# Kernel optimization log

Measured on AMD Instinct MI355X. Metric: run time of the kernel, lower is better.

The kernel has to match this reference:

```python
import jax, jax.numpy as jnp
import numpy as np

SMALL_CONST = 1e-8
K = 128
N = 512 * 512  # pixels


def setup_inputs() -> dict:
    key = jax.random.key(0)
    ks = jax.random.split(key, 6)
    pos = jax.random.uniform(ks[0], (N, 2), jnp.float32, 0.0, 512.0)      # pixel coords
    mu = jax.random.uniform(ks[1], (K, 2), jnp.float32, 0.0, 512.0)       # gaussian centers
    alpha = jax.random.uniform(ks[2], (K,), jnp.float32)                   # opacities in [0,1]
    color = jax.random.uniform(ks[3], (K, 3), jnp.float32, 0.0, 255.0)     # RGB in [0,255]
    scales = 10.0 + jax.random.uniform(ks[4], (K, 2), jnp.float32) * 20.0  # anisotropic scales
    thetas = jax.random.uniform(ks[5], (K,), jnp.float32, -np.pi, np.pi)   # rotations
    return dict(pos=pos, mu=mu, alpha=alpha, color=color, scales=scales, thetas=thetas)


def _forward(pos, mu, alpha, color, scales, thetas):
    # Parameter clamps done at the top of the torch forward
    alpha = jnp.clip(alpha, 0.0, 1.0)
    color = jnp.clip(color, 0.0, 255.0)
    scales = jnp.clip(scales, 0.1, None)

    # Precompute all K inverse covariances: sigma_inv = R diag(1/s^2) R^T  -> [K,2,2]
    c, s = jnp.cos(thetas), jnp.sin(thetas)
    R = jnp.stack([jnp.stack([c, -s], -1), jnp.stack([s, c], -1)], -2)  # [K,2,2]
    inv2 = 1.0 / scales ** 2                                            # [K,2]
    sigma_inv = jnp.einsum('kti,ki,kji->ktj', R, inv2, R)               # [K,2,2]

    n = pos.shape[0]
    pc0 = jnp.zeros((n, 3), pos.dtype)
    pa0 = jnp.zeros((n, 1), pos.dtype)

    def step(carry, g):
        pc, pa = carry
        mu_k, si_k, a_k, col_k = g
        diff = pos - mu_k                                          # [N,2]
        expo = -0.5 * jnp.einsum('ni,ij,nj->n', diff, si_k, diff)  # [N]
        alpha_k = (a_k * jnp.exp(expo))[:, None]                   # [N,1]
        new_alpha = pa + alpha_k * (1.0 - pa)
        pc = (pc * pa + col_k * alpha_k * (1.0 - pa)) / (new_alpha + SMALL_CONST)
        pc = jnp.clip(pc, 0.0, 255.0)
        pa = jnp.clip(new_alpha, 0.0, 1.0)
        return (pc, pa), None

    (pc, pa), _ = jax.lax.scan(jax.checkpoint(step), (pc0, pa0),
                               (mu, sigma_inv, alpha, color))
    # include_opc=True path: append alpha channel scaled to [0,255]
    return jnp.concatenate([pc, pa * 255.0], axis=-1)  # [N,4]


def reference(pos, mu, alpha, color, scales, thetas):
    return _forward(pos, mu, alpha, color, scales, thetas)
```

## Files before the change

kernel.cpp:

```cpp
#include <hip/hip_runtime.h>
#include <math.h>

#define KG 128

typedef float f32x2 __attribute__((ext_vector_type(2)));

__global__ __launch_bounds__(256) void splat_fwd(
    const float* __restrict__ pos,
    const float* __restrict__ mu,
    const float* __restrict__ alpha,
    const float* __restrict__ color,
    const float* __restrict__ scales,
    const float* __restrict__ thetas,
    float* __restrict__ out,
    int nPairs)
{
    __shared__ float4 sP0[KG];
    __shared__ float4 sP1[KG];
    __shared__ float  sP2[KG];

    const int tid = threadIdx.x;
    if (tid < KG) {
        const int k = tid;
        const float mx = mu[2 * k];
        const float my = mu[2 * k + 1];
        const float al = fminf(fmaxf(alpha[k], 0.0f), 1.0f);
        const float cr = fminf(fmaxf(color[3 * k + 0], 0.0f), 255.0f);
        const float cg = fminf(fmaxf(color[3 * k + 1], 0.0f), 255.0f);
        const float cb = fminf(fmaxf(color[3 * k + 2], 0.0f), 255.0f);
        const float sx = fmaxf(scales[2 * k + 0], 0.1f);
        const float sy = fmaxf(scales[2 * k + 1], 0.1f);
        const float th = thetas[k];
        const float c = cosf(th);
        const float s = sinf(th);
        const float i0 = 1.0f / (sx * sx);
        const float i1 = 1.0f / (sy * sy);
        const float a  = c * c * i0 + s * s * i1;
        const float b  = c * s * (i0 - i1);
        const float cc = s * s * i0 + c * c * i1;
        const float f = -0.5f * 1.4426950408889634f;
        sP0[k] = make_float4(mx, my, a * f, 2.0f * b * f);
        sP1[k] = make_float4(cc * f, al, cr, cg);
        sP2[k] = cb;
    }
    __syncthreads();

    const int t = blockIdx.x * blockDim.x + tid;
    if (t >= nPairs) return;

    const float4 pp = reinterpret_cast<const float4*>(pos)[t];
    const f32x2 px = { pp.x, pp.z };
    const f32x2 py = { pp.y, pp.w };

    f32x2 pa    = { 0.0f, 0.0f };
    f32x2 rprev = { 0.0f, 0.0f };
    f32x2 numr  = { 0.0f, 0.0f };
    f32x2 numg  = { 0.0f, 0.0f };
    f32x2 numb  = { 0.0f, 0.0f };

#pragma unroll 4
    for (int k = 0; k < KG; ++k) {
        const float4 q0 = sP0[k];
        const float4 q1 = sP1[k];
        const float  q2 = sP2[k];

        const f32x2 dx = px - q0.x;
        const f32x2 dy = py - q0.y;
        const f32x2 u  = q0.z * dx + q0.w * dy;
        const f32x2 e  = dx * u + (q1.x * dy) * dy;

        f32x2 E;
        E.x = __builtin_amdgcn_exp2f(e.x);
        E.y = __builtin_amdgcn_exp2f(e.y);

        const f32x2 w   = q1.y * E;
        const f32x2 omp = 1.0f - pa;
        const f32x2 t1  = w * omp;
        const f32x2 na  = pa + t1;
        const f32x2 nae = na + 1e-8f;

        f32x2 r;
        r.x = __builtin_amdgcn_rcpf(nae.x);
        r.y = __builtin_amdgcn_rcpf(nae.y);

        const f32x2 h = rprev * pa;
        numr = numr * h + q1.z * t1;
        numg = numg * h + q1.w * t1;
        numb = numb * h + q2  * t1;

        pa.x = fminf(na.x, 1.0f);
        pa.y = fminf(na.y, 1.0f);
        rprev = r;
    }

    const f32x2 pcr = numr * rprev;
    const f32x2 pcg = numg * rprev;
    const f32x2 pcb = numb * rprev;

    float4 o0, o1;
    o0.x = fminf(fmaxf(pcr.x, 0.0f), 255.0f);
    o0.y = fminf(fmaxf(pcg.x, 0.0f), 255.0f);
    o0.z = fminf(fmaxf(pcb.x, 0.0f), 255.0f);
    o0.w = pa.x * 255.0f;
    o1.x = fminf(fmaxf(pcr.y, 0.0f), 255.0f);
    o1.y = fminf(fmaxf(pcg.y, 0.0f), 255.0f);
    o1.z = fminf(fmaxf(pcb.y, 0.0f), 255.0f);
    o1.w = pa.y * 255.0f;

    float4* o = reinterpret_cast<float4*>(out);
    o[2 * t]     = o0;
    o[2 * t + 1] = o1;
}

extern "C" void kernel_launch(void* const* d_in, const int* in_sizes, int n_in,
                              void* d_out, int out_size, void* d_ws, size_t ws_size,
                              hipStream_t stream) {
    const float* pos    = (const float*)d_in[0];
    const float* mu     = (const float*)d_in[1];
    const float* alpha  = (const float*)d_in[2];
    const float* color  = (const float*)d_in[3];
    const float* scales = (const float*)d_in[4];
    const float* thetas = (const float*)d_in[5];
    float* out = (float*)d_out;

    const int n = in_sizes[0] / 2;
    const int nPairs = n / 2;
    const int block = 256;
    const int grid = (nPairs + block - 1) / block;
    hipLaunchKernelGGL(splat_fwd, dim3(grid), dim3(block), 0, stream,
                       pos, mu, alpha, color, scales, thetas, out, nPairs);
}
```

Measured before the change: 81.55 us.

## Split parameter precompute into separate kernel and read params from global memory

Moves the per-Gaussian parameter setup (trig, inverse covariance, clamps) out of every block into a single-block precompute kernel that writes to workspace. The main kernel then drops shared memory and the block barrier, reading uniform parameters straight from global memory, which may become scalar loads through the constant cache. This removes redundant per-block trig work and the sync, but adds a second kernel launch and a dependency between the two kernels.

```diff
diff --git a/kernel.cpp b/kernel.cpp
--- a/kernel.cpp
+++ b/kernel.cpp
@@ -5,47 +5,49 @@
 
 typedef float f32x2 __attribute__((ext_vector_type(2)));
 
-__global__ __launch_bounds__(256) void splat_fwd(
-    const float* __restrict__ pos,
+__global__ __launch_bounds__(128) void precompute_params(
     const float* __restrict__ mu,
     const float* __restrict__ alpha,
     const float* __restrict__ color,
     const float* __restrict__ scales,
     const float* __restrict__ thetas,
+    float4* __restrict__ P0,
+    float4* __restrict__ P1,
+    float*  __restrict__ P2)
+{
+    const int k = threadIdx.x;
+    if (k >= KG) return;
+    const float mx = mu[2 * k];
+    const float my = mu[2 * k + 1];
+    const float al = fminf(fmaxf(alpha[k], 0.0f), 1.0f);
+    const float cr = fminf(fmaxf(color[3 * k + 0], 0.0f), 255.0f);
+    const float cg = fminf(fmaxf(color[3 * k + 1], 0.0f), 255.0f);
+    const float cb = fminf(fmaxf(color[3 * k + 2], 0.0f), 255.0f);
+    const float sx = fmaxf(scales[2 * k + 0], 0.1f);
+    const float sy = fmaxf(scales[2 * k + 1], 0.1f);
+    const float th = thetas[k];
+    const float c = cosf(th);
+    const float s = sinf(th);
+    const float i0 = 1.0f / (sx * sx);
+    const float i1 = 1.0f / (sy * sy);
+    const float a  = c * c * i0 + s * s * i1;
+    const float b  = c * s * (i0 - i1);
+    const float cc = s * s * i0 + c * c * i1;
+    const float f = -0.5f * 1.4426950408889634f;
+    P0[k] = make_float4(mx, my, a * f, 2.0f * b * f);
+    P1[k] = make_float4(cc * f, al, cr, cg);
+    P2[k] = cb;
+}
+
+__global__ __launch_bounds__(256) void splat_fwd(
+    const float* __restrict__ pos,
+    const float4* __restrict__ P0,
+    const float4* __restrict__ P1,
+    const float*  __restrict__ P2,
     float* __restrict__ out,
     int nPairs)
 {
-    __shared__ float4 sP0[KG];
-    __shared__ float4 sP1[KG];
-    __shared__ float  sP2[KG];
-
-    const int tid = threadIdx.x;
-    if (tid < KG) {
-        const int k = tid;
-        const float mx = mu[2 * k];
-        const float my = mu[2 * k + 1];
-        const float al = fminf(fmaxf(alpha[k], 0.0f), 1.0f);
-        const float cr = fminf(fmaxf(color[3 * k + 0], 0.0f), 255.0f);
-        const float cg = fminf(fmaxf(color[3 * k + 1], 0.0f), 255.0f);
-        const float cb = fminf(fmaxf(color[3 * k + 2], 0.0f), 255.0f);
-        const float sx = fmaxf(scales[2 * k + 0], 0.1f);
-        const float sy = fmaxf(scales[2 * k + 1], 0.1f);
-        const float th = thetas[k];
-        const float c = cosf(th);
-        const float s = sinf(th);
-        const float i0 = 1.0f / (sx * sx);
-        const float i1 = 1.0f / (sy * sy);
-        const float a  = c * c * i0 + s * s * i1;
-        const float b  = c * s * (i0 - i1);
-        const float cc = s * s * i0 + c * c * i1;
-        const float f = -0.5f * 1.4426950408889634f;
-        sP0[k] = make_float4(mx, my, a * f, 2.0f * b * f);
-        sP1[k] = make_float4(cc * f, al, cr, cg);
-        sP2[k] = cb;
-    }
-    __syncthreads();
-
-    const int t = blockIdx.x * blockDim.x + tid;
+    const int t = blockIdx.x * blockDim.x + threadIdx.x;
     if (t >= nPairs) return;
 
     const float4 pp = reinterpret_cast<const float4*>(pos)[t];
@@ -60,9 +62,9 @@
 
 #pragma unroll 4
     for (int k = 0; k < KG; ++k) {
-        const float4 q0 = sP0[k];
-        const float4 q1 = sP1[k];
-        const float  q2 = sP2[k];
+        const float4 q0 = P0[k];
+        const float4 q1 = P1[k];
+        const float  q2 = P2[k];
 
         const f32x2 dx = px - q0.x;
         const f32x2 dy = py - q0.y;
@@ -123,10 +125,17 @@
     const float* thetas = (const float*)d_in[5];
     float* out = (float*)d_out;
 
+    float4* P0 = (float4*)d_ws;
+    float4* P1 = P0 + KG;
+    float*  P2 = (float*)(P1 + KG);
+
     const int n = in_sizes[0] / 2;
     const int nPairs = n / 2;
     const int block = 256;
     const int grid = (nPairs + block - 1) / block;
+
+    hipLaunchKernelGGL(precompute_params, dim3(1), dim3(128), 0, stream,
+                       mu, alpha, color, scales, thetas, P0, P1, P2);
     hipLaunchKernelGGL(splat_fwd, dim3(grid), dim3(block), 0, stream,
-                       pos, mu, alpha, color, scales, thetas, out, nPairs);
+                       pos, P0, P1, P2, out, nPairs);
 }
```

New measurement: 83.70 us. 1.03x slower.
